# Kernel optimization log

Measured on AMD Instinct MI355X. Metric: run time of the kernel, lower is better.

Reference implementation:

```python
import jax, jax.numpy as jnp
import numpy as np

D, H, F, NL, B, TT, TS = 1024, 16, 4096, 4, 16, 128, 512
HD = D // H
NEG = -1e9


def layer_norm(x, s, b):
    m = x.mean(-1, keepdims=True)
    v = ((x - m) ** 2).mean(-1, keepdims=True)
    return (x - m) * jax.lax.rsqrt(v + 1e-5) * s + b


def setup_inputs() -> dict:
    key = jax.random.key(0)
    ks = jax.random.split(key, 28)
    text_encoded = jax.random.normal(ks[0], (TT, B, D), jnp.float32)
    speech_encoded = jax.random.normal(ks[1], (TS, B, D), jnp.float32)
    tlen = jax.random.randint(ks[2], (B,), 32, TT + 1)
    slen = jax.random.randint(ks[3], (B,), 128, TS + 1)
    text_padding_mask = jnp.arange(TT)[None, :] >= tlen[:, None]
    speech_padding_mask = jnp.arange(TS)[None, :] >= slen[:, None]
    sc = 0.02
    p = lambda k, sh: jax.random.normal(k, sh, jnp.float32) * sc
    return dict(
        text_encoded=text_encoded, speech_encoded=speech_encoded,
        text_padding_mask=text_padding_mask, speech_padding_mask=speech_padding_mask,
        cls_vector=p(ks[4], (D,)), sep_vector=p(ks[5], (D,)),
        Wq=p(ks[6], (NL, D, D)), bq=jnp.zeros((NL, D)),
        Wk=p(ks[7], (NL, D, D)), bk=jnp.zeros((NL, D)),
        Wv=p(ks[8], (NL, D, D)), bv=jnp.zeros((NL, D)),
        Wo=p(ks[9], (NL, D, D)), bo=jnp.zeros((NL, D)),
        ln1_s=jnp.ones((NL, D)), ln1_b=jnp.zeros((NL, D)),
        fc1_w=p(ks[10], (NL, D, F)), fc1_b=jnp.zeros((NL, F)),
        fc2_w=p(ks[11], (NL, F, D)), fc2_b=jnp.zeros((NL, D)),
        ln2_s=jnp.ones((NL, D)), ln2_b=jnp.zeros((NL, D)),
        out_w=p(ks[12], (1, D)),
    )


def _forward(text_encoded, speech_encoded, text_padding_mask, speech_padding_mask,
             cls_vector, sep_vector, Wq, bq, Wk, bk, Wv, bv, Wo, bo,
             ln1_s, ln1_b, fc1_w, fc1_b, fc2_w, fc2_b, ln2_s, ln2_b, out_w):
    Tt, Bb, d = text_encoded.shape
    Ts = speech_encoded.shape[0]
    L = Tt + Ts + 2  # static max concat length
    tlen = (~text_padding_mask).sum(-1)[:, None]   # [B,1]
    slen = (~speech_padding_mask).sum(-1)[:, None]  # [B,1]
    pos = jnp.arange(L)[None, :]                    # [1,L]
    is_cls = pos == 0
    is_text = (pos >= 1) & (pos < 1 + tlen)
    is_sep = pos == 1 + tlen
    is_speech = (pos >= 2 + tlen) & (pos < 2 + tlen + slen)
    # fused gather into the padded [B, L, D] buffer (replaces per-batch cat loop)
    text_bf = jnp.swapaxes(text_encoded, 0, 1)      # [B,Tt,D]
    speech_bf = jnp.swapaxes(speech_encoded, 0, 1)  # [B,Ts,D]
    t_idx = jnp.clip(pos - 1, 0, Tt - 1)
    s_idx = jnp.clip(pos - 2 - tlen, 0, Ts - 1)
    g_t = jnp.take_along_axis(text_bf, jnp.broadcast_to(t_idx[..., None], (Bb, L, 1)), axis=1)
    g_s = jnp.take_along_axis(speech_bf, jnp.broadcast_to(s_idx[..., None], (Bb, L, 1)), axis=1)
    x = jnp.where(is_cls[..., None], cls_vector,
        jnp.where(is_text[..., None], g_t,
        jnp.where(is_sep[..., None], sep_vector,
        jnp.where(is_speech[..., None], g_s, jnp.zeros((), x1 := text_encoded.dtype)))))  # [B,L,D]
    pad_mask = pos >= (2 + tlen + slen)             # [B,L] True = pad

    scale = HD ** -0.5
    for l in range(NL):  # post-norm fairseq encoder layers
        q = (x @ Wq[l] + bq[l]).reshape(Bb, L, H, HD) * scale
        k = (x @ Wk[l] + bk[l]).reshape(Bb, L, H, HD)
        v = (x @ Wv[l] + bv[l]).reshape(Bb, L, H, HD)
        scores = jnp.einsum('bqhd,bkhd->bhqk', q, k)
        scores = jnp.where(pad_mask[:, None, None, :], NEG, scores)
        attn = jax.nn.softmax(scores, axis=-1)
        o = jnp.einsum('bhqk,bkhd->bqhd', attn, v).reshape(Bb, L, D)
        x = layer_norm(x + (o @ Wo[l] + bo[l]), ln1_s[l], ln1_b[l])
        h = jax.nn.relu(x @ fc1_w[l] + fc1_b[l])
        x = layer_norm(x + (h @ fc2_w[l] + fc2_b[l]), ln2_s[l], ln2_b[l])
    return x[:, 0, :] @ out_w.T  # [B,1]


def reference(text_encoded, speech_encoded, text_padding_mask, speech_padding_mask,
              cls_vector, sep_vector, Wq, bq, Wk, bk, Wv, bv, Wo, bo,
              ln1_s, ln1_b, fc1_w, fc1_b, fc2_w, fc2_b, ln2_s, ln2_b, out_w):
    return _forward(text_encoded, speech_encoded, text_padding_mask, speech_padding_mask,
                    cls_vector, sep_vector, Wq, bq, Wk, bk, Wv, bv, Wo, bo,
                    ln1_s, ln1_b, fc1_w, fc1_b, fc2_w, fc2_b, ln2_s, ln2_b, out_w)
```

## Files before the change

### kernel.cpp

```cpp
#include <hip/hip_runtime.h>
#include <hip/hip_bf16.h>
#include <stdint.h>

#define D_   1024
#define H_   16
#define HD_  64
#define F_   4096
#define NL_  4
#define B_   16
#define TT_  128
#define TS_  512
#define LP_  704
#define M_   (B_*LP_)

typedef __attribute__((ext_vector_type(8)))  __bf16 bf16x8;
typedef __attribute__((ext_vector_type(4)))  float  floatx4;

typedef __attribute__((address_space(3))) void lds_void_t;
typedef const __attribute__((address_space(1))) void g_void_t;

__device__ __forceinline__ void gl2lds16(const __bf16* g, const __bf16* l) {
  __builtin_amdgcn_global_load_lds((g_void_t*)g, (lds_void_t*)l, 16, 0, 0);
}

__global__ void lens_kernel(const int* __restrict__ tmask, const int* __restrict__ smask,
                            int* __restrict__ lens) {
  __shared__ int red[256];
  int b = blockIdx.x, t = threadIdx.x;
  int tc = 0, sc = 0;
  if (t < TT_) tc = (tmask[b*TT_ + t] == 0) ? 1 : 0;
  for (int i = t; i < TS_; i += 256) sc += (smask[b*TS_ + i] == 0) ? 1 : 0;
  red[t] = tc + (sc << 16);
  __syncthreads();
  for (int s = 128; s > 0; s >>= 1) {
    if (t < s) red[t] += red[t + s];
    __syncthreads();
  }
  if (t == 0) {
    int tl = red[0] & 0xffff, sl = red[0] >> 16;
    if (tl < 0) tl = 0; if (tl > TT_) tl = TT_;
    if (sl < 0) sl = 0; if (sl > TS_) sl = TS_;
    int Lb = 2 + tl + sl;
    if (Lb > LP_) Lb = LP_;
    lens[2*b] = tl; lens[2*b+1] = Lb;
  }
}

__global__ void plan_kernel(const int* __restrict__ lens, int* __restrict__ plan) {
  if (threadIdx.x == 0 && blockIdx.x == 0) {
    int off = 0;
    for (int b = 0; b < B_; b++) {
      plan[2 + b] = off;
      int Lb = lens[2*b+1];
      int pad = ((Lb + 127) >> 7) << 7;
      if (pad > LP_) pad = LP_;
      off += pad;
    }
    plan[2 + B_] = off;
    plan[1] = off;
    plan[0] = (off + 127) >> 7;
  }
}

__global__ void transpose_kernel(const float* __restrict__ in, __bf16* __restrict__ out,
                                 int R, int C) {
  __shared__ float tile[32][33];
  int x = threadIdx.x & 31, y0 = threadIdx.x >> 5;
  const float* inb = in + (size_t)blockIdx.z * R * C;
  __bf16* outb = out + (size_t)blockIdx.z * R * C;
  int r0 = blockIdx.y * 32, c0 = blockIdx.x * 32;
  #pragma unroll
  for (int i = 0; i < 4; i++) {
    int y = y0 + 8*i;
    tile[y][x] = inb[(size_t)(r0 + y)*C + c0 + x];
  }
  __syncthreads();
  #pragma unroll
  for (int i = 0; i < 4; i++) {
    int y = y0 + 8*i;
    outb[(size_t)(c0 + y)*R + r0 + x] = (__bf16)tile[x][y];
  }
}

__global__ void build_x_kernel(const float* __restrict__ text, const float* __restrict__ speech,
                               const float* __restrict__ cls, const float* __restrict__ sep,
                               const int* __restrict__ lens, const int* __restrict__ plan,
                               __bf16* __restrict__ xbf) {
  int b = blockIdx.y, l = blockIdx.x;
  int off = plan[2+b], padLb = plan[3+b] - off;
  if (l >= padLb) return;
  int tl = lens[2*b], Lb = lens[2*b+1];
  const float* src = nullptr;
  if (l == 0)              src = cls;
  else if (l <= tl)        src = text   + ((size_t)(l-1)*B_ + b)*D_;
  else if (l == tl + 1)    src = sep;
  else if (l < Lb)         src = speech + ((size_t)(l-2-tl)*B_ + b)*D_;
  __bf16* dst = xbf + (size_t)(off + l) * D_;
  #pragma unroll
  for (int j = 0; j < 4; j++) {
    int i = threadIdx.x + j*256;
    float v = src ? src[i] : 0.f;
    dst[i] = (__bf16)v;
  }
}

template<int MODE>
__global__ __launch_bounds__(256, 2)
void gemm_kernel(const __bf16* __restrict__ A, const __bf16* __restrict__ BT,
                 const float* __restrict__ bias, void* __restrict__ Cv,
                 const int* __restrict__ plan, int Nn, int Kk, float scale) {
  if ((int)blockIdx.y >= plan[0]) return;
  __shared__ __bf16 As[128*32];
  __shared__ __bf16 Bs[128*32];
  int tid = threadIdx.x;
  int w = tid >> 6, l = tid & 63;
  int wm = w >> 1, wn = w & 1;
  long tile_m = (long)blockIdx.y * 128;
  long tile_n = (long)blockIdx.x * 128;

  floatx4 acc[4][4] = {};

  const __bf16* ga = A  + (tile_m + w*32 + (l>>2)) * (long)Kk + (l&3)*8;
  const __bf16* gb = BT + (tile_n + w*32 + (l>>2)) * (long)Kk + (l&3)*8;
  const __bf16* lA = As + (w*32)*32;
  const __bf16* lB = Bs + (w*32)*32;

  int kcol = (l >> 4) * 8;
  const __bf16* afp = As + (wm*64 + (l&15))*32 + kcol;
  const __bf16* bfp = Bs + (wn*64 + (l&15))*32 + kcol;

  for (int k0 = 0; k0 < Kk; k0 += 32) {
    gl2lds16(ga,              lA);
    gl2lds16(ga + 16*(long)Kk, lA + 16*32);
    gl2lds16(gb,              lB);
    gl2lds16(gb + 16*(long)Kk, lB + 16*32);
    ga += 32; gb += 32;
    __syncthreads();
    bf16x8 af[4], bf[4];
    #pragma unroll
    for (int mi = 0; mi < 4; mi++) af[mi] = *(const bf16x8*)(afp + mi*16*32);
    #pragma unroll
    for (int ni = 0; ni < 4; ni++) bf[ni] = *(const bf16x8*)(bfp + ni*16*32);
    #pragma unroll
    for (int mi = 0; mi < 4; mi++)
      #pragma unroll
      for (int ni = 0; ni < 4; ni++)
        acc[mi][ni] = __builtin_amdgcn_mfma_f32_16x16x32_bf16(af[mi], bf[ni], acc[mi][ni], 0, 0, 0);
    __syncthreads();
  }

  int rbase = wm*64 + (l>>4)*4;
  int cbase = wn*64 + (l&15);
  #pragma unroll
  for (int mi = 0; mi < 4; mi++) {
    long row0 = tile_m + rbase + mi*16;
    long voff = 0;
    int bb = 0;
    if (MODE == 4) {
      #pragma unroll
      for (int t = 1; t < B_; t++) bb += (row0 >= plan[2+t]) ? 1 : 0;
      voff = plan[2+bb];
    }
    #pragma unroll
    for (int ni = 0; ni < 4; ni++) {
      long col = tile_n + cbase + ni*16;
      float bv = bias[col];
      #pragma unroll
      for (int r = 0; r < 4; r++) {
        long row = row0 + r;
        float v = acc[mi][ni][r] + bv;
        if (MODE == 3) v *= scale;
        if (MODE == 2) v = v > 0.f ? v : 0.f;
        if (MODE == 0)      ((float*)Cv)[row*Nn + col] = v;
        else if (MODE == 4) {
          long ll = row - voff;
          if (ll < LP_)
            ((__bf16*)Cv)[(((long)bb*H_ + (col>>6))*HD_ + (col&63))*LP_ + ll] = (__bf16)v;
        }
        else                ((__bf16*)Cv)[row*Nn + col] = (__bf16)v;
      }
    }
  }
}

__global__ __launch_bounds__(256, 2)
void attn_kernel(const __bf16* __restrict__ qb, const __bf16* __restrict__ kb,
                 const __bf16* __restrict__ vt, __bf16* __restrict__ ob,
                 const int* __restrict__ lens, const int* __restrict__ plan) {
  int col = blockIdx.x;
  int b = col >> 4;
  int off = plan[2+b];
  int padLb = plan[3+b] - off;
  if ((int)blockIdx.y * 128 >= padLb) return;
  __shared__ __bf16 Ks[64*64];
  __shared__ __bf16 Vs[64*64];
  __shared__ __bf16 Ps[4][32*72];
  int tid = threadIdx.x, w = tid >> 6, l = tid & 63;
  int Lb = lens[2*b+1];
  int q0w = blockIdx.y*128 + w*32;
  const size_t bh  = (size_t)off*D_ + (size_t)(col & 15)*HD_;
  const size_t vtb = (size_t)col * HD_ * LP_;
  int nkt = (Lb + 63) >> 6;

  bf16x8 qf[2][2];
  #pragma unroll
  for (int mi = 0; mi < 2; mi++) {
    int qr = q0w + mi*16 + (l&15);
    if (qr > padLb-1) qr = padLb-1;
    const __bf16* qp = qb + bh + (size_t)qr*D_ + (l>>4)*8;
    qf[mi][0] = *(const bf16x8*)(qp);
    qf[mi][1] = *(const bf16x8*)(qp + 32);
  }
  bf16x8 ones;
  #pragma unroll
  for (int j = 0; j < 8; j++) ones[j] = (__bf16)1.0f;

  floatx4 oacc[2][4] = {};
  floatx4 lacc[2] = {};

  for (int kt = 0; kt < nkt; kt++) {
    int kbase = kt*64;
    {
      int krow = w*16 + (l>>3);
      int cb = (l&7) ^ (krow & 7);
      const __bf16* gk = kb + bh + (size_t)(kbase + krow)*D_ + cb*8;
      const __bf16* lk = Ks + (w*16)*64;
      gl2lds16(gk,                lk);
      gl2lds16(gk + 8*(size_t)D_, lk + 8*64);
    }
    {
      int vrow = w*8 + (l>>3);
      int sb = (l&7) ^ (l>>3);
      const __bf16* gv = vt + vtb + (size_t)vrow*LP_ + kbase + sb*8;
      const __bf16* lv = Vs + (w*8)*64;
      gl2lds16(gv,                  lv);
      gl2lds16(gv + 32*(size_t)LP_, lv + 32*64);
    }
    __syncthreads();

    floatx4 s4[2][4] = {};
    #pragma unroll
    for (int ks = 0; ks < 2; ks++) {
      #pragma unroll
      for (int ni = 0; ni < 4; ni++) {
        int n = ni*16 + (l&15);
        int blk = (ks*4 + (l>>4)) ^ (n & 7);
        bf16x8 kf = *(const bf16x8*)(Ks + n*64 + blk*8);
        s4[0][ni] = __builtin_amdgcn_mfma_f32_16x16x32_bf16(qf[0][ks], kf, s4[0][ni], 0, 0, 0);
        s4[1][ni] = __builtin_amdgcn_mfma_f32_16x16x32_bf16(qf[1][ks], kf, s4[1][ni], 0, 0, 0);
      }
    }
    #pragma unroll
    for (int mi = 0; mi < 2; mi++) {
      #pragma unroll
      for (int ni = 0; ni < 4; ni++) {
        int key = kbase + ni*16 + (l&15);
        bool valid = key < Lb;
        #pragma unroll
        for (int r = 0; r < 4; r++) {
          float sv = valid ? fminf(s4[mi][ni][r], 30.f) : -1e9f;
          float p = __expf(sv);
          Ps[w][(mi*16 + (l>>4)*4 + r)*72 + ni*16 + (l&15)] = (__bf16)p;
        }
      }
    }
    #pragma unroll
    for (int ks = 0; ks < 2; ks++) {
      bf16x8 pf0 = *(const bf16x8*)(&Ps[w][(l&15)*72 + ks*32 + (l>>4)*8]);
      bf16x8 pf1 = *(const bf16x8*)(&Ps[w][(16 + (l&15))*72 + ks*32 + (l>>4)*8]);
      lacc[0] = __builtin_amdgcn_mfma_f32_16x16x32_bf16(pf0, ones, lacc[0], 0, 0, 0);
      lacc[1] = __builtin_amdgcn_mfma_f32_16x16x32_bf16(pf1, ones, lacc[1], 0, 0, 0);
      #pragma unroll
      for (int ni = 0; ni < 4; ni++) {
        int n = ni*16 + (l&15);
        int blk = (ks*4 + (l>>4)) ^ (n & 7);
        bf16x8 vf = *(const bf16x8*)(Vs + n*64 + blk*8);
        oacc[0][ni] = __builtin_amdgcn_mfma_f32_16x16x32_bf16(pf0, vf, oacc[0][ni], 0, 0, 0);
        oacc[1][ni] = __builtin_amdgcn_mfma_f32_16x16x32_bf16(pf1, vf, oacc[1][ni], 0, 0, 0);
      }
    }
    __syncthreads();
  }

  #pragma unroll
  for (int mi = 0; mi < 2; mi++) {
    #pragma unroll
    for (int ni = 0; ni < 4; ni++) {
      #pragma unroll
      for (int r = 0; r < 4; r++) {
        int qrow = q0w + mi*16 + (l>>4)*4 + r;
        if (qrow < padLb) {
          float ov = oacc[mi][ni][r] / lacc[mi][r];
          ob[bh + (size_t)qrow*D_ + ni*16 + (l&15)] = (__bf16)ov;
        }
      }
    }
  }
}

__global__ void ln_kernel(__bf16* __restrict__ x, const float* __restrict__ t,
                          const float* __restrict__ sc, const float* __restrict__ bi,
                          const int* __restrict__ plan) {
  int row = blockIdx.x;
  if (row >= plan[1]) return;
  __shared__ float red[2][4];
  int tid = threadIdx.x;
  const float* tr = t + (size_t)row * D_;
  __bf16* xr = x + (size_t)row * D_;
  float v[4], s1 = 0.f, s2 = 0.f;
  #pragma unroll
  for (int j = 0; j < 4; j++) {
    int i = tid + j*256;
    float val = (float)xr[i] + tr[i];
    v[j] = val; s1 += val; s2 += val*val;
  }
  #pragma unroll
  for (int off = 1; off < 64; off <<= 1) {
    s1 += __shfl_xor(s1, off, 64);
    s2 += __shfl_xor(s2, off, 64);
  }
  int w = tid >> 6, l = tid & 63;
  if (l == 0) { red[0][w] = s1; red[1][w] = s2; }
  __syncthreads();
  s1 = red[0][0] + red[0][1] + red[0][2] + red[0][3];
  s2 = red[1][0] + red[1][1] + red[1][2] + red[1][3];
  float mean = s1 * (1.f/D_);
  float var  = s2 * (1.f/D_) - mean*mean;
  float rstd = rsqrtf(var + 1e-5f);
  #pragma unroll
  for (int j = 0; j < 4; j++) {
    int i = tid + j*256;
    xr[i] = (__bf16)((v[j] - mean)*rstd*sc[i] + bi[i]);
  }
}

__global__ void out_kernel(const __bf16* __restrict__ x, const float* __restrict__ wv,
                           const int* __restrict__ plan, float* __restrict__ out) {
  __shared__ float red[4];
  int b = blockIdx.x, tid = threadIdx.x;
  const __bf16* xr = x + (size_t)plan[2+b] * D_;
  float s = 0.f;
  #pragma unroll
  for (int j = 0; j < 4; j++) {
    int i = tid + j*256;
    s += (float)xr[i] * wv[i];
  }
  #pragma unroll
  for (int off = 1; off < 64; off <<= 1) s += __shfl_xor(s, off, 64);
  int w = tid >> 6, l = tid & 63;
  if (l == 0) red[w] = s;
  __syncthreads();
  if (tid == 0) out[b] = red[0] + red[1] + red[2] + red[3];
}

extern "C" void kernel_launch(void* const* d_in, const int* in_sizes, int n_in,
                              void* d_out, int out_size, void* d_ws, size_t ws_size,
                              hipStream_t stream) {
  (void)in_sizes; (void)n_in; (void)out_size; (void)ws_size;
  const float* text   = (const float*)d_in[0];
  const float* speech = (const float*)d_in[1];
  const int*   tmask  = (const int*)d_in[2];
  const int*   smask  = (const int*)d_in[3];
  const float* cls    = (const float*)d_in[4];
  const float* sep    = (const float*)d_in[5];
  const float* Wq     = (const float*)d_in[6];
  const float* bq     = (const float*)d_in[7];
  const float* Wk     = (const float*)d_in[8];
  const float* bk     = (const float*)d_in[9];
  const float* Wv     = (const float*)d_in[10];
  const float* bv     = (const float*)d_in[11];
  const float* Wo     = (const float*)d_in[12];
  const float* bo     = (const float*)d_in[13];
  const float* ln1s   = (const float*)d_in[14];
  const float* ln1b   = (const float*)d_in[15];
  const float* fc1w   = (const float*)d_in[16];
  const float* fc1b   = (const float*)d_in[17];
  const float* fc2w   = (const float*)d_in[18];
  const float* fc2b   = (const float*)d_in[19];
  const float* ln2s   = (const float*)d_in[20];
  const float* ln2b   = (const float*)d_in[21];
  const float* outw   = (const float*)d_in[22];

  const size_t MD = (size_t)M_ * D_;
  char* ws = (char*)d_ws;
  int*    lens = (int*)ws;
  int*    plan = (int*)(ws + 128);
  __bf16* xbf  = (__bf16*)(ws + 256);
  __bf16* act  = (__bf16*)(ws + 256 + MD*2);
  float*  tmp  = (float*) (ws + 256 + MD*2 + 4*MD*2);
  __bf16* wt   = (__bf16*)(ws + 256 + MD*2 + 4*MD*2 + MD*4);

  __bf16* qb   = act;
  __bf16* kb   = act + MD;
  __bf16* vtG  = act + 2*MD;
  __bf16* obuf = act + 3*MD;
  __bf16* hb   = act;

  const size_t DD = (size_t)D_*D_;
  const size_t DF = (size_t)D_*F_;
  __bf16* wqT  = wt;
  __bf16* wkT  = wt + 4*DD;
  __bf16* wvT  = wt + 8*DD;
  __bf16* woT  = wt + 12*DD;
  __bf16* fc1T = wt + 16*DD;
  __bf16* fc2T = wt + 16*DD + 4*DF;

  lens_kernel<<<B_, 256, 0, stream>>>(tmask, smask, lens);
  plan_kernel<<<1, 64, 0, stream>>>(lens, plan);

  transpose_kernel<<<dim3(D_/32, D_/32, NL_), 256, 0, stream>>>(Wq, wqT, D_, D_);
  transpose_kernel<<<dim3(D_/32, D_/32, NL_), 256, 0, stream>>>(Wk, wkT, D_, D_);
  transpose_kernel<<<dim3(D_/32, D_/32, NL_), 256, 0, stream>>>(Wv, wvT, D_, D_);
  transpose_kernel<<<dim3(D_/32, D_/32, NL_), 256, 0, stream>>>(Wo, woT, D_, D_);
  transpose_kernel<<<dim3(F_/32, D_/32, NL_), 256, 0, stream>>>(fc1w, fc1T, D_, F_);
  transpose_kernel<<<dim3(D_/32, F_/32, NL_), 256, 0, stream>>>(fc2w, fc2T, F_, D_);

  build_x_kernel<<<dim3(LP_, B_), 256, 0, stream>>>(text, speech, cls, sep, lens, plan, xbf);

  for (int lyr = 0; lyr < NL_; lyr++) {
    gemm_kernel<3><<<dim3(D_/128, M_/128), 256, 0, stream>>>(xbf, wqT + lyr*DD, bq + lyr*D_, qb, plan, D_, D_, 0.125f);
    gemm_kernel<1><<<dim3(D_/128, M_/128), 256, 0, stream>>>(xbf, wkT + lyr*DD, bk + lyr*D_, kb, plan, D_, D_, 1.f);
    gemm_kernel<4><<<dim3(D_/128, M_/128), 256, 0, stream>>>(xbf, wvT + lyr*DD, bv + lyr*D_, vtG, plan, D_, D_, 1.f);
    attn_kernel<<<dim3(B_*H_, (LP_+127)/128), 256, 0, stream>>>(qb, kb, vtG, obuf, lens, plan);
    gemm_kernel<0><<<dim3(D_/128, M_/128), 256, 0, stream>>>(obuf, woT + lyr*DD, bo + lyr*D_, tmp, plan, D_, D_, 1.f);
    ln_kernel<<<M_, 256, 0, stream>>>(xbf, tmp, ln1s + lyr*D_, ln1b + lyr*D_, plan);
    gemm_kernel<2><<<dim3(F_/128, M_/128), 256, 0, stream>>>(xbf, fc1T + lyr*DF, fc1b + lyr*F_, hb, plan, F_, D_, 1.f);
    gemm_kernel<0><<<dim3(D_/128, M_/128), 256, 0, stream>>>(hb, fc2T + lyr*DF, fc2b + lyr*D_, tmp, plan, D_, F_, 1.f);
    ln_kernel<<<M_, 256, 0, stream>>>(xbf, tmp, ln2s + lyr*D_, ln2b + lyr*D_, plan);
  }

  out_kernel<<<B_, 256, 0, stream>>>(xbf, outw, plan, (float*)d_out);
}
```

Measured before the change: 1.787 ms.

## Fuse QKV projections into one GEMM and split-K the fc2 GEMM

Lays out the Q, K and V weights as one interleaved transposed matrix per layer so a single GEMM launch with a 3072-wide N produces Q (scaled), K, and head-transposed V through a segment-aware epilogue. The fc2 GEMM is split along K into four z-slices that atomically add fp32 partial sums into a buffer; the first LayerNorm pre-fills that buffer with the fc2 bias. The goal is fewer launches and more blocks in flight for the narrow-N, long-K fc2 GEMM. The cost is fp32 atomic traffic, and the sum order is no longer deterministic.

```diff
diff --git a/kernel.cpp b/kernel.cpp
--- a/kernel.cpp
+++ b/kernel.cpp
@@ -63,11 +63,11 @@
 }
 
 __global__ void transpose_kernel(const float* __restrict__ in, __bf16* __restrict__ out,
-                                 int R, int C) {
+                                 int R, int C, long ozs) {
   __shared__ float tile[32][33];
   int x = threadIdx.x & 31, y0 = threadIdx.x >> 5;
   const float* inb = in + (size_t)blockIdx.z * R * C;
-  __bf16* outb = out + (size_t)blockIdx.z * R * C;
+  __bf16* outb = out + (size_t)blockIdx.z * ozs;
   int r0 = blockIdx.y * 32, c0 = blockIdx.x * 32;
   #pragma unroll
   for (int i = 0; i < 4; i++) {
@@ -107,8 +107,9 @@
 template<int MODE>
 __global__ __launch_bounds__(256, 2)
 void gemm_kernel(const __bf16* __restrict__ A, const __bf16* __restrict__ BT,
-                 const float* __restrict__ bias, void* __restrict__ Cv,
-                 const int* __restrict__ plan, int Nn, int Kk, float scale) {
+                 const float* __restrict__ bias, const float* __restrict__ bias2,
+                 const float* __restrict__ bias3, void* __restrict__ Cv,
+                 const int* __restrict__ plan, int Nn, int Kk, int Kloop, float scale) {
   if ((int)blockIdx.y >= plan[0]) return;
   __shared__ __bf16 As[128*32];
   __shared__ __bf16 Bs[128*32];
@@ -117,11 +118,12 @@
   int wm = w >> 1, wn = w & 1;
   long tile_m = (long)blockIdx.y * 128;
   long tile_n = (long)blockIdx.x * 128;
+  long koff = (MODE == 6) ? (long)blockIdx.z * Kloop : 0;
 
   floatx4 acc[4][4] = {};
 
-  const __bf16* ga = A  + (tile_m + w*32 + (l>>2)) * (long)Kk + (l&3)*8;
-  const __bf16* gb = BT + (tile_n + w*32 + (l>>2)) * (long)Kk + (l&3)*8;
+  const __bf16* ga = A  + (tile_m + w*32 + (l>>2)) * (long)Kk + (l&3)*8 + koff;
+  const __bf16* gb = BT + (tile_n + w*32 + (l>>2)) * (long)Kk + (l&3)*8 + koff;
   const __bf16* lA = As + (w*32)*32;
   const __bf16* lB = Bs + (w*32)*32;
 
@@ -129,10 +131,10 @@
   const __bf16* afp = As + (wm*64 + (l&15))*32 + kcol;
   const __bf16* bfp = Bs + (wn*64 + (l&15))*32 + kcol;
 
-  for (int k0 = 0; k0 < Kk; k0 += 32) {
-    gl2lds16(ga,              lA);
+  for (int k0 = 0; k0 < Kloop; k0 += 32) {
+    gl2lds16(ga,               lA);
     gl2lds16(ga + 16*(long)Kk, lA + 16*32);
-    gl2lds16(gb,              lB);
+    gl2lds16(gb,               lB);
     gl2lds16(gb + 16*(long)Kk, lB + 16*32);
     ga += 32; gb += 32;
     __syncthreads();
@@ -151,12 +153,13 @@
 
   int rbase = wm*64 + (l>>4)*4;
   int cbase = wn*64 + (l&15);
+  int seg = (int)(tile_n >> 10);
   #pragma unroll
   for (int mi = 0; mi < 4; mi++) {
     long row0 = tile_m + rbase + mi*16;
     long voff = 0;
     int bb = 0;
-    if (MODE == 4) {
+    if (MODE == 5) {
       #pragma unroll
       for (int t = 1; t < B_; t++) bb += (row0 >= plan[2+t]) ? 1 : 0;
       voff = plan[2+bb];
@@ -164,18 +167,32 @@
     #pragma unroll
     for (int ni = 0; ni < 4; ni++) {
       long col = tile_n + cbase + ni*16;
-      float bv = bias[col];
+      float bv;
+      if (MODE == 5) {
+        const float* bp = (seg == 0) ? bias : (seg == 1) ? bias2 : bias3;
+        bv = bp[col & 1023];
+      } else if (MODE == 6) {
+        bv = 0.f;
+      } else {
+        bv = bias[col];
+      }
       #pragma unroll
       for (int r = 0; r < 4; r++) {
         long row = row0 + r;
         float v = acc[mi][ni][r] + bv;
-        if (MODE == 3) v *= scale;
         if (MODE == 2) v = v > 0.f ? v : 0.f;
         if (MODE == 0)      ((float*)Cv)[row*Nn + col] = v;
-        else if (MODE == 4) {
-          long ll = row - voff;
-          if (ll < LP_)
-            ((__bf16*)Cv)[(((long)bb*H_ + (col>>6))*HD_ + (col&63))*LP_ + ll] = (__bf16)v;
+        else if (MODE == 6) atomicAdd(&((float*)Cv)[row*Nn + col], v);
+        else if (MODE == 5) {
+          __bf16* base = (__bf16*)Cv;
+          long c = col & 1023;
+          if (seg == 0)       base[row*D_ + c] = (__bf16)(v * scale);
+          else if (seg == 1)  base[(long)M_*D_ + row*D_ + c] = (__bf16)v;
+          else {
+            long ll = row - voff;
+            if (ll < LP_)
+              base[2L*M_*D_ + (((long)bb*H_ + (c>>6))*HD_ + (c&63))*LP_ + ll] = (__bf16)v;
+          }
         }
         else                ((__bf16*)Cv)[row*Nn + col] = (__bf16)v;
       }
@@ -300,7 +317,8 @@
 
 __global__ void ln_kernel(__bf16* __restrict__ x, const float* __restrict__ t,
                           const float* __restrict__ sc, const float* __restrict__ bi,
-                          const int* __restrict__ plan) {
+                          const int* __restrict__ plan,
+                          float* __restrict__ pre, const float* __restrict__ preb) {
   int row = blockIdx.x;
   if (row >= plan[1]) return;
   __shared__ float red[2][4];
@@ -331,6 +349,7 @@
   for (int j = 0; j < 4; j++) {
     int i = tid + j*256;
     xr[i] = (__bf16)((v[j] - mean)*rstd*sc[i] + bi[i]);
+    if (pre) pre[(size_t)row*D_ + i] = preb[i];
   }
 }
 
@@ -398,35 +417,38 @@
 
   const size_t DD = (size_t)D_*D_;
   const size_t DF = (size_t)D_*F_;
-  __bf16* wqT  = wt;
-  __bf16* wkT  = wt + 4*DD;
-  __bf16* wvT  = wt + 8*DD;
-  __bf16* woT  = wt + 12*DD;
-  __bf16* fc1T = wt + 16*DD;
-  __bf16* fc2T = wt + 16*DD + 4*DF;
+  __bf16* wqkvT = wt;
+  __bf16* woT   = wt + 12*DD;
+  __bf16* fc1T  = wt + 16*DD;
+  __bf16* fc2T  = wt + 16*DD + 4*DF;
 
   lens_kernel<<<B_, 256, 0, stream>>>(tmask, smask, lens);
   plan_kernel<<<1, 64, 0, stream>>>(lens, plan);
 
-  transpose_kernel<<<dim3(D_/32, D_/32, NL_), 256, 0, stream>>>(Wq, wqT, D_, D_);
-  transpose_kernel<<<dim3(D_/32, D_/32, NL_), 256, 0, stream>>>(Wk, wkT, D_, D_);
-  transpose_kernel<<<dim3(D_/32, D_/32, NL_), 256, 0, stream>>>(Wv, wvT, D_, D_);
-  transpose_kernel<<<dim3(D_/32, D_/32, NL_), 256, 0, stream>>>(Wo, woT, D_, D_);
-  transpose_kernel<<<dim3(F_/32, D_/32, NL_), 256, 0, stream>>>(fc1w, fc1T, D_, F_);
-  transpose_kernel<<<dim3(D_/32, F_/32, NL_), 256, 0, stream>>>(fc2w, fc2T, F_, D_);
+  transpose_kernel<<<dim3(D_/32, D_/32, NL_), 256, 0, stream>>>(Wq, wqkvT,        D_, D_, 3*DD);
+  transpose_kernel<<<dim3(D_/32, D_/32, NL_), 256, 0, stream>>>(Wk, wqkvT + DD,   D_, D_, 3*DD);
+  transpose_kernel<<<dim3(D_/32, D_/32, NL_), 256, 0, stream>>>(Wv, wqkvT + 2*DD, D_, D_, 3*DD);
+  transpose_kernel<<<dim3(D_/32, D_/32, NL_), 256, 0, stream>>>(Wo, woT,  D_, D_, DD);
+  transpose_kernel<<<dim3(F_/32, D_/32, NL_), 256, 0, stream>>>(fc1w, fc1T, D_, F_, DF);
+  transpose_kernel<<<dim3(D_/32, F_/32, NL_), 256, 0, stream>>>(fc2w, fc2T, F_, D_, DF);
 
   build_x_kernel<<<dim3(LP_, B_), 256, 0, stream>>>(text, speech, cls, sep, lens, plan, xbf);
 
   for (int lyr = 0; lyr < NL_; lyr++) {
-    gemm_kernel<3><<<dim3(D_/128, M_/128), 256, 0, stream>>>(xbf, wqT + lyr*DD, bq + lyr*D_, qb, plan, D_, D_, 0.125f);
-    gemm_kernel<1><<<dim3(D_/128, M_/128), 256, 0, stream>>>(xbf, wkT + lyr*DD, bk + lyr*D_, kb, plan, D_, D_, 1.f);
-    gemm_kernel<4><<<dim3(D_/128, M_/128), 256, 0, stream>>>(xbf, wvT + lyr*DD, bv + lyr*D_, vtG, plan, D_, D_, 1.f);
+    gemm_kernel<5><<<dim3(24, M_/128), 256, 0, stream>>>(
+        xbf, wqkvT + (size_t)lyr*3*DD, bq + lyr*D_, bk + lyr*D_, bv + lyr*D_,
+        act, plan, 3072, D_, D_, 0.125f);
     attn_kernel<<<dim3(B_*H_, (LP_+127)/128), 256, 0, stream>>>(qb, kb, vtG, obuf, lens, plan);
-    gemm_kernel<0><<<dim3(D_/128, M_/128), 256, 0, stream>>>(obuf, woT + lyr*DD, bo + lyr*D_, tmp, plan, D_, D_, 1.f);
-    ln_kernel<<<M_, 256, 0, stream>>>(xbf, tmp, ln1s + lyr*D_, ln1b + lyr*D_, plan);
-    gemm_kernel<2><<<dim3(F_/128, M_/128), 256, 0, stream>>>(xbf, fc1T + lyr*DF, fc1b + lyr*F_, hb, plan, F_, D_, 1.f);
-    gemm_kernel<0><<<dim3(D_/128, M_/128), 256, 0, stream>>>(hb, fc2T + lyr*DF, fc2b + lyr*D_, tmp, plan, D_, F_, 1.f);
-    ln_kernel<<<M_, 256, 0, stream>>>(xbf, tmp, ln2s + lyr*D_, ln2b + lyr*D_, plan);
+    gemm_kernel<0><<<dim3(D_/128, M_/128), 256, 0, stream>>>(
+        obuf, woT + (size_t)lyr*DD, bo + lyr*D_, nullptr, nullptr, tmp, plan, D_, D_, D_, 1.f);
+    ln_kernel<<<M_, 256, 0, stream>>>(xbf, tmp, ln1s + lyr*D_, ln1b + lyr*D_, plan,
+                                      tmp, fc2b + lyr*D_);
+    gemm_kernel<2><<<dim3(F_/128, M_/128), 256, 0, stream>>>(
+        xbf, fc1T + (size_t)lyr*DF, fc1b + lyr*F_, nullptr, nullptr, hb, plan, F_, D_, D_, 1.f);
+    gemm_kernel<6><<<dim3(D_/128, M_/128, 4), 256, 0, stream>>>(
+        hb, fc2T + (size_t)lyr*DF, nullptr, nullptr, nullptr, tmp, plan, D_, F_, 1024, 1.f);
+    ln_kernel<<<M_, 256, 0, stream>>>(xbf, tmp, ln2s + lyr*D_, ln2b + lyr*D_, plan,
+                                      nullptr, nullptr);
   }
 
   out_kernel<<<B_, 256, 0, stream>>>(xbf, outw, plan, (float*)d_out);
```

New measurement: 1.921 ms. 1.08x slower.
